# Kernel optimization log

Measured on AMD Instinct MI355X. Metric: run time of the kernel, lower is better.

The kernel has to match this reference:

```python
import jax, jax.numpy as jnp
import numpy as np

silu = jax.nn.silu

B, N, E, H, T, L, A = 8, 20000, 40000, 128, 64, 4, 4


def setup_inputs() -> dict:
    key = jax.random.key(0)
    ks = jax.random.split(key, 20)
    s = 0.05
    w = lambda k, shape: jax.random.normal(k, shape, jnp.float32) * s
    return {
        "x": jax.random.normal(ks[0], (B, N, 3), jnp.float32),
        "t": jax.random.uniform(ks[1], (B,), jnp.float32) * 1000.0,
        "atom_types": jax.random.randint(ks[2], (N,), 0, A),
        "bond_indices": jax.random.randint(ks[3], (E, 2), 0, N),
        "emb_table": w(ks[4], (A, H)),
        "W_t1": w(ks[5], (T, H)), "b_t1": jnp.zeros((H,), jnp.float32),
        "W_t2": w(ks[6], (H, H)), "b_t2": jnp.zeros((H,), jnp.float32),
        "W_node": w(ks[7], (H, H)), "b_node": jnp.zeros((H,), jnp.float32),
        "Wm1": w(ks[8], (L, 2 * H + 1, H)), "bm1": jnp.zeros((L, H), jnp.float32),
        "Wm2": w(ks[9], (L, H, H)), "bm2": jnp.zeros((L, H), jnp.float32),
        "Wn1": w(ks[10], (L, 2 * H, H)), "bn1": jnp.zeros((L, H), jnp.float32),
        "Wn2": w(ks[11], (L, H, H)), "bn2": jnp.zeros((L, H), jnp.float32),
        "Wc1": w(ks[12], (L, H, H)), "bc1": jnp.zeros((L, H), jnp.float32),
        "Wc2": w(ks[13], (L, H, 1)) * 0.001,  # xavier gain=0.001 final coord layer
        "W_o1": w(ks[14], (H, H)), "b_o1": jnp.zeros((H,), jnp.float32),
        "W_o2": w(ks[15], (H, 3)), "b_o2": jnp.zeros((3,), jnp.float32),
    }


def reference(x, t, atom_types, bond_indices, emb_table,
              W_t1, b_t1, W_t2, b_t2, W_node, b_node,
              Wm1, bm1, Wm2, bm2, Wn1, bn1, Wn2, bn2, Wc1, bc1, Wc2,
              W_o1, b_o1, W_o2, b_o2):
    n_atoms = x.shape[1]
    src = bond_indices[:, 0]
    dst = bond_indices[:, 1]

    # sinusoidal time embedding -> time MLP
    half = W_t1.shape[0] // 2
    freq = jnp.exp(jnp.arange(half, dtype=jnp.float32) * (-np.log(10000.0) / (half - 1)))
    te = t[:, None] * freq[None, :]
    te = jnp.concatenate([jnp.sin(te), jnp.cos(te)], axis=-1)  # [B, T]
    t_emb = silu(te @ W_t1 + b_t1) @ W_t2 + b_t2  # [B, H]

    # node init: embedding -> linear -> + time emb
    h0 = emb_table[atom_types] @ W_node + b_node  # [N, H]
    h = h0[None, :, :] + t_emb[:, None, :]  # [B, N, H]

    # degree counts (src+dst incidence), clamped to >=1
    ones = jnp.ones((src.shape[0],), jnp.float32)
    counts = jnp.zeros((n_atoms,), jnp.float32).at[dst].add(ones).at[src].add(ones)
    counts = jnp.maximum(counts, 1.0)

    x_orig = x
    n_layers = Wm1.shape[0]
    for l in range(n_layers):
        h_src = h[:, src, :]
        h_dst = h[:, dst, :]
        coord_diff = x[:, dst, :] - x[:, src, :]  # [B, E, 3]
        dist = jnp.sqrt(jnp.sum(coord_diff * coord_diff, axis=-1, keepdims=True))
        msg_in = jnp.concatenate([h_src, h_dst, dist], axis=-1)  # [B, E, 2H+1]
        m = silu(msg_in @ Wm1[l] + bm1[l])
        m = silu(m @ Wm2[l] + bm2[l])  # [B, E, H]

        agg = jnp.zeros_like(h).at[:, dst, :].add(m).at[:, src, :].add(m)
        h_in = jnp.concatenate([h, agg], axis=-1)
        h = h + silu(h_in @ Wn1[l] + bn1[l]) @ Wn2[l] + bn2[l]

        cw = silu(m @ Wc1[l] + bc1[l]) @ Wc2[l]  # [B, E, 1]
        cdn = coord_diff / (dist + 1e-8)
        upd = cdn * cw
        coord_update = jnp.zeros_like(x).at[:, dst, :].add(upd).at[:, src, :].add(-upd)
        x = x + coord_update / counts[None, :, None]

    coord_change = x - x_orig
    noise_from_h = silu(h @ W_o1 + b_o1) @ W_o2 + b_o2
    return coord_change + noise_from_h
```

## Files before the change

kernel.cpp:

```cpp
#include <hip/hip_runtime.h>
#include <math.h>

#define B_ 8
#define N_ 20000
#define E_ 40000
#define H_ 128
#define L_ 4
#define A_ 4
#define MRS 136
#define EPB 64
#define NPB 64

#define WFENCE __asm__ __volatile__("" ::: "memory")

typedef _Float16 f16x8 __attribute__((ext_vector_type(8)));
typedef _Float16 f16x4v __attribute__((ext_vector_type(4)));
typedef float f32x4 __attribute__((ext_vector_type(4)));

__device__ __forceinline__ float silu_f(float x) {
    return x * __builtin_amdgcn_rcpf(1.f + __expf(-x));
}


__global__ void k_zero(int* __restrict__ deg, int* __restrict__ cursor) {
    int i = blockIdx.x * 256 + threadIdx.x;
    if (i < N_) { deg[i] = 0; cursor[i] = 0; }
}

__global__ void k_deg(const int* __restrict__ bond, int* __restrict__ deg) {
    int e = blockIdx.x * 256 + threadIdx.x;
    if (e < E_) {
        atomicAdd(&deg[bond[2 * e]], 1);
        atomicAdd(&deg[bond[2 * e + 1]], 1);
    }
}

__global__ void k_scan(const int* __restrict__ deg, int* __restrict__ indptr) {
    __shared__ int sums[1024];
    const int CH = (N_ + 1023) / 1024;
    int t = threadIdx.x;
    int s0 = t * CH;
    int s1 = min(s0 + CH, N_);
    int s = 0;
    for (int i = s0; i < s1; ++i) s += deg[i];
    sums[t] = s;
    __syncthreads();
    for (int off = 1; off < 1024; off <<= 1) {
        int v = (t >= off) ? sums[t - off] : 0;
        __syncthreads();
        sums[t] += v;
        __syncthreads();
    }
    int base = (t > 0) ? sums[t - 1] : 0;
    int run = base;
    for (int i = s0; i < s1; ++i) { indptr[i] = run; run += deg[i]; }
    if (s1 == N_ && s0 < N_) indptr[N_] = run;
}

__global__ void k_fill(const int* __restrict__ bond, const int* __restrict__ indptr,
                       int* __restrict__ cursor, int* __restrict__ adj) {
    int e = blockIdx.x * 256 + threadIdx.x;
    if (e < E_) {
        int s = bond[2 * e], d = bond[2 * e + 1];
        int ps = indptr[s] + atomicAdd(&cursor[s], 1);
        adj[ps] = (e << 1);
        int pd = indptr[d] + atomicAdd(&cursor[d], 1);
        adj[pd] = (e << 1) | 1;
    }
}

__global__ void k_wprepL(const float* __restrict__ W, _Float16* __restrict__ Wf,
                         int K, int wstride) {
    int l = blockIdx.y;
    const float* Wl = W + (size_t)l * wstride;
    _Float16* Wfl = Wf + (size_t)l * K * 128;
    int idx = blockIdx.x * 256 + threadIdx.x;
    if (idx >= K * 128) return;
    int j = idx & 7, lane = (idx >> 3) & 63, nt = (idx >> 9) & 7, kt = idx >> 12;
    int k = kt * 32 + (lane >> 4) * 8 + j;
    int n = nt * 16 + (lane & 15);
    Wfl[idx] = (_Float16)Wl[k * 128 + n];
}

__global__ void k_temb(const float* __restrict__ tv,
                       const float* __restrict__ W1, const float* __restrict__ b1,
                       const float* __restrict__ W2, const float* __restrict__ b2,
                       float* __restrict__ t_emb) {
    __shared__ float te[64];
    __shared__ float h1[128];
    int b = blockIdx.x;
    int tid = threadIdx.x;
    float tval = tv[b];
    if (tid < 32) {
        float fr = __expf((float)tid * (-logf(10000.f) / 31.f));
        float a = tval * fr;
        te[tid] = sinf(a);
        te[tid + 32] = cosf(a);
    }
    __syncthreads();
    float acc = b1[tid];
    for (int k = 0; k < 64; ++k) acc += te[k] * W1[k * 128 + tid];
    h1[tid] = silu_f(acc);
    __syncthreads();
    float acc2 = b2[tid];
    for (int k = 0; k < 128; ++k) acc2 += h1[k] * W2[k * 128 + tid];
    t_emb[b * 128 + tid] = acc2;
}

__global__ void k_embproj(const float* __restrict__ emb, const float* __restrict__ W,
                          const float* __restrict__ bias, float* __restrict__ outp) {
    int tid = threadIdx.x;
    int a = tid >> 7, j = tid & 127;
    float acc = bias[j];
    for (int k = 0; k < 128; ++k) acc += emb[a * 128 + k] * W[k * 128 + j];
    outp[a * 128 + j] = acc;
}

__global__ void k_hinit(const int* __restrict__ at, const float* __restrict__ embp,
                        const float* __restrict__ temb, float* __restrict__ h,
                        _Float16* __restrict__ h16) {
    size_t idx4 = (size_t)blockIdx.x * 256 + threadIdx.x;
    size_t e0 = idx4 * 4;
    int j = (int)(e0 % H_);
    size_t bn = e0 / H_;
    int n = (int)(bn % N_);
    int b = (int)(bn / N_);
    int a = at[n];
    float4 ep = *(const float4*)(embp + a * H_ + j);
    float4 tv = *(const float4*)(temb + b * H_ + j);
    float4 r = make_float4(ep.x + tv.x, ep.y + tv.y, ep.z + tv.z, ep.w + tv.w);
    ((float4*)h)[idx4] = r;
    f16x4v o;
    o[0] = (_Float16)r.x; o[1] = (_Float16)r.y; o[2] = (_Float16)r.z; o[3] = (_Float16)r.w;
    *(f16x4v*)(h16 + e0) = o;
}

__global__ void k_xcopy(const float* __restrict__ x, float* __restrict__ xb) {
    int i = blockIdx.x * 256 + threadIdx.x;
    xb[i] = x[i];
}

template <int RS, int KT>
__device__ __forceinline__ void mfma_gemm(const _Float16* Asw, const _Float16* __restrict__ Wf,
                                          f32x4 (&acc)[8], int ml, int quad, int lane) {
    #pragma unroll
    for (int kt = 0; kt < KT; ++kt) {
        f16x8 a = *(const f16x8*)(Asw + ml * RS + kt * 32 + quad * 8);
        #pragma unroll
        for (int nt = 0; nt < 8; ++nt) {
            f16x8 b = *(const f16x8*)(Wf + (((kt * 8 + nt) * 64 + lane) * 8));
            acc[nt] = __builtin_amdgcn_mfma_f32_16x16x32_f16(a, b, acc[nt], 0, 0, 0);
        }
    }
}

template <int RS, int KT>
__device__ __forceinline__ void mfma_gemm2(const _Float16* Asw, const _Float16* __restrict__ Wf,
                                           f32x4 (&acc)[2][8], int ml, int quad, int lane) {
    #pragma unroll
    for (int kt = 0; kt < KT; ++kt) {
        f16x8 a0 = *(const f16x8*)(Asw + ml * RS + kt * 32 + quad * 8);
        f16x8 a1 = *(const f16x8*)(Asw + (16 + ml) * RS + kt * 32 + quad * 8);
        #pragma unroll
        for (int nt = 0; nt < 8; ++nt) {
            f16x8 b = *(const f16x8*)(Wf + (((kt * 8 + nt) * 64 + lane) * 8));
            acc[0][nt] = __builtin_amdgcn_mfma_f32_16x16x32_f16(a0, b, acc[0][nt], 0, 0, 0);
            acc[1][nt] = __builtin_amdgcn_mfma_f32_16x16x32_f16(a1, b, acc[1][nt], 0, 0, 0);
        }
    }
}

__device__ __forceinline__ void load_row(f16x8 (&v)[4], const _Float16* mp) {
    #pragma unroll
    for (int j = 0; j < 4; ++j) v[j] = *(const f16x8*)(mp + j * 8);
}
__device__ __forceinline__ void acc_row(float (&ag)[4][8], const f16x8 (&v)[4]) {
    #pragma unroll
    for (int j = 0; j < 4; ++j)
        #pragma unroll
        for (int i = 0; i < 8; ++i) ag[j][i] += (float)v[j][i];
}


__global__ __launch_bounds__(128, 3) void k_edge_mfma(
    const _Float16* __restrict__ h16, const float* __restrict__ xcur,
    const int* __restrict__ bond,
    const float* __restrict__ Wm1, const float* __restrict__ bm1,
    const _Float16* __restrict__ Wm1f,
    const float* __restrict__ bm2, const _Float16* __restrict__ Wm2f,
    const float* __restrict__ bc1, const _Float16* __restrict__ Wc1f,
    const float* __restrict__ Wc2,
    _Float16* __restrict__ m16, float* __restrict__ upd) {
    __shared__ _Float16 As[EPB * MRS];
    __shared__ float ds_s[EPB];
    __shared__ float dx_s[EPB], dy_s[EPB], dz_s[EPB];
    int tid = threadIdx.x;
    int b = blockIdx.x & 7;
    int e0 = (blockIdx.x >> 3) * EPB;
    size_t be0 = (size_t)b * E_ + e0;

    int el = tid >> 1, q = tid & 1;
    int2 sd = ((const int2*)bond)[e0 + el];
    int s = sd.x, d = sd.y;

    const _Float16* hs = h16 + ((size_t)b * N_ + s) * H_ + q * 64;
    const _Float16* hd = h16 + ((size_t)b * N_ + d) * H_ + q * 64;
    f16x8 ps[8], pd[8];
    #pragma unroll
    for (int j = 0; j < 8; ++j) ps[j] = *(const f16x8*)(hs + j * 8);
    #pragma unroll
    for (int j = 0; j < 8; ++j) pd[j] = *(const f16x8*)(hd + j * 8);
    if (q == 0) {
        const float* xs = xcur + ((size_t)b * N_ + s) * 3;
        const float* xd = xcur + ((size_t)b * N_ + d) * 3;
        float dx = xd[0] - xs[0], dy = xd[1] - xs[1], dz = xd[2] - xs[2];
        ds_s[el] = sqrtf(dx * dx + dy * dy + dz * dz);
        dx_s[el] = dx; dy_s[el] = dy; dz_s[el] = dz;
    }
    {
        _Float16* ap = As + el * MRS + q * 64;
        #pragma unroll
        for (int j = 0; j < 8; ++j) *(f16x8*)(ap + j * 8) = ps[j];
    }
    WFENCE;

    int lane = tid & 63, w = tid >> 6;
    int ml = lane & 15, quad = lane >> 4;
    _Float16* Asw = As + w * 32 * MRS;
    const float* wd = Wm1 + 256 * H_;

    f32x4 acc[2][8];
    #pragma unroll
    for (int nt = 0; nt < 8; ++nt) {
        int col = nt * 16 + ml;
        float bb = bm1[col];
        float ww = wd[col];
        #pragma unroll
        for (int rt = 0; rt < 2; ++rt)
            #pragma unroll
            for (int r = 0; r < 4; ++r)
                acc[rt][nt][r] = bb + ds_s[w * 32 + rt * 16 + quad * 4 + r] * ww;
    }
    mfma_gemm2<MRS, 4>(Asw, Wm1f, acc, ml, quad, lane);
    WFENCE;
    {
        _Float16* ap = As + el * MRS + q * 64;
        #pragma unroll
        for (int j = 0; j < 8; ++j) *(f16x8*)(ap + j * 8) = pd[j];
    }
    WFENCE;
    mfma_gemm2<MRS, 4>(Asw, Wm1f + 4 * 8 * 64 * 8, acc, ml, quad, lane);
    WFENCE;
    #pragma unroll
    for (int rt = 0; rt < 2; ++rt)
        #pragma unroll
        for (int nt = 0; nt < 8; ++nt)
            #pragma unroll
            for (int r = 0; r < 4; ++r)
                Asw[(rt * 16 + quad * 4 + r) * MRS + nt * 16 + ml] = (_Float16)silu_f(acc[rt][nt][r]);
    WFENCE;

    #pragma unroll
    for (int nt = 0; nt < 8; ++nt) {
        float bb = bm2[nt * 16 + ml];
        #pragma unroll
        for (int rt = 0; rt < 2; ++rt)
            #pragma unroll
            for (int r = 0; r < 4; ++r) acc[rt][nt][r] = bb;
    }
    mfma_gemm2<MRS, 4>(Asw, Wm2f, acc, ml, quad, lane);
    WFENCE;
    #pragma unroll
    for (int rt = 0; rt < 2; ++rt)
        #pragma unroll
        for (int nt = 0; nt < 8; ++nt)
            #pragma unroll
            for (int r = 0; r < 4; ++r)
                Asw[(rt * 16 + quad * 4 + r) * MRS + nt * 16 + ml] = (_Float16)silu_f(acc[rt][nt][r]);
    WFENCE;
    #pragma unroll
    for (int j = 0; j < 8; ++j)
        *(f16x8*)(m16 + (be0 + el) * H_ + q * 64 + j * 8) =
            *(const f16x8*)(As + el * MRS + q * 64 + j * 8);

    #pragma unroll
    for (int nt = 0; nt < 8; ++nt) {
        float bb = bc1[nt * 16 + ml];
        #pragma unroll
        for (int rt = 0; rt < 2; ++rt)
            #pragma unroll
            for (int r = 0; r < 4; ++r) acc[rt][nt][r] = bb;
    }
    mfma_gemm2<MRS, 4>(Asw, Wc1f, acc, ml, quad, lane);
    float part[2][4] = {{0.f, 0.f, 0.f, 0.f}, {0.f, 0.f, 0.f, 0.f}};
    #pragma unroll
    for (int nt = 0; nt < 8; ++nt) {
        float wv = Wc2[nt * 16 + ml];
        #pragma unroll
        for (int rt = 0; rt < 2; ++rt)
            #pragma unroll
            for (int r = 0; r < 4; ++r) part[rt][r] += silu_f(acc[rt][nt][r]) * wv;
    }
    #pragma unroll
    for (int off = 1; off < 16; off <<= 1)
        #pragma unroll
        for (int rt = 0; rt < 2; ++rt)
            #pragma unroll
            for (int r = 0; r < 4; ++r) part[rt][r] += __shfl_xor(part[rt][r], off, 64);
    if (ml < 3) {
        #pragma unroll
        for (int rt = 0; rt < 2; ++rt)
            #pragma unroll
            for (int r = 0; r < 4; ++r) {
                int ee = w * 32 + rt * 16 + quad * 4 + r;
                float wv = part[rt][r] * __builtin_amdgcn_rcpf(ds_s[ee] + 1e-8f);
                float comp = (ml == 0) ? dx_s[ee] : ((ml == 1) ? dy_s[ee] : dz_s[ee]);
                upd[(be0 + ee) * 3 + ml] = comp * wv;
            }
    }
}

__global__ void k_coord(const float* __restrict__ xcur, float* __restrict__ xnext,
                        const float* __restrict__ upd,
                        const int* __restrict__ indptr, const int* __restrict__ adj) {
    int idx = blockIdx.x * 256 + threadIdx.x;
    int b = idx / N_;
    int n = idx - b * N_;
    const float* ub = upd + (size_t)b * E_ * 3;
    int p0 = indptr[n], p1 = indptr[n + 1];
    float ax = 0.f, ay = 0.f, az = 0.f;
    for (int p = p0; p < p1; ++p) {
        int a = adj[p];
        int e = a >> 1;
        float sgn = (a & 1) ? 1.f : -1.f;
        ax += sgn * ub[e * 3 + 0];
        ay += sgn * ub[e * 3 + 1];
        az += sgn * ub[e * 3 + 2];
    }
    float rcnt = __builtin_amdgcn_rcpf((float)max(p1 - p0, 1));
    xnext[(size_t)idx * 3 + 0] = xcur[(size_t)idx * 3 + 0] + ax * rcnt;
    xnext[(size_t)idx * 3 + 1] = xcur[(size_t)idx * 3 + 1] + ay * rcnt;
    xnext[(size_t)idx * 3 + 2] = xcur[(size_t)idx * 3 + 2] + az * rcnt;
}

__global__ __launch_bounds__(256, 4) void k_node_mfma(
    float* __restrict__ h, _Float16* __restrict__ h16,
    const _Float16* __restrict__ m16,
    const int* __restrict__ indptr, const int* __restrict__ adj,
    const float* __restrict__ bn1, const _Float16* __restrict__ Wn1f,
    const float* __restrict__ bn2, const _Float16* __restrict__ Wn2f) {
    __shared__ _Float16 As[NPB * MRS];
    int tid = threadIdx.x;
    int el = tid >> 2, q = tid & 3;
    int be = blockIdx.x * NPB + el;
    int b = be / N_, n = be - b * N_;
    {
        const _Float16* hr = h16 + (size_t)be * H_;
        #pragma unroll
        for (int j = 0; j < 4; ++j)
            *(f16x8*)(As + el * MRS + q * 32 + j * 8) = *(const f16x8*)(hr + q * 32 + j * 8);
    }
    int p0 = indptr[n], p1 = indptr[n + 1];
    int d0 = p1 - p0;
    const _Float16* mbb = m16 + (size_t)b * E_ * H_;
    int ea = (d0 > 0) ? (adj[p0] >> 1) : 0;
    int eb = (d0 > 1) ? (adj[p0 + 1] >> 1) : ea;
    f16x8 va[4], vb[4];
    load_row(va, mbb + (size_t)ea * H_ + q * 32);
    load_row(vb, mbb + (size_t)eb * H_ + q * 32);
    WFENCE;

    int lane = tid & 63, w = tid >> 6;
    int ml = lane & 15, quad = lane >> 4;
    _Float16* Asw = As + w * 16 * MRS;
    size_t be0 = (size_t)blockIdx.x * NPB;

    f32x4 acc[8];
    #pragma unroll
    for (int nt = 0; nt < 8; ++nt) {
        float bb = bn1[nt * 16 + ml];
        #pragma unroll
        for (int r = 0; r < 4; ++r) acc[nt][r] = bb;
    }
    mfma_gemm<MRS, 4>(Asw, Wn1f, acc, ml, quad, lane);
    WFENCE;
    {
        float ag[4][8];
        #pragma unroll
        for (int j = 0; j < 4; ++j)
            #pragma unroll
            for (int i = 0; i < 8; ++i) ag[j][i] = 0.f;
        if (d0 > 0) acc_row(ag, va);
        if (d0 > 1) acc_row(ag, vb);
        int p = p0 + 2;
        while (p + 2 <= p1) {
            int e1 = adj[p] >> 1, e2 = adj[p + 1] >> 1;
            f16x8 w1[4], w2[4];
            load_row(w1, mbb + (size_t)e1 * H_ + q * 32);
            load_row(w2, mbb + (size_t)e2 * H_ + q * 32);
            acc_row(ag, w1);
            acc_row(ag, w2);
            p += 2;
        }
        if (p < p1) {
            int e1 = adj[p] >> 1;
            f16x8 w1[4];
            load_row(w1, mbb + (size_t)e1 * H_ + q * 32);
            acc_row(ag, w1);
        }
        #pragma unroll
        for (int j = 0; j < 4; ++j) {
            f16x8 o;
            #pragma unroll
            for (int i = 0; i < 8; ++i) o[i] = (_Float16)ag[j][i];
            *(f16x8*)(As + el * MRS + q * 32 + j * 8) = o;
        }
    }
    WFENCE;
    mfma_gemm<MRS, 4>(Asw, Wn1f + 4 * 8 * 64 * 8, acc, ml, quad, lane);
    WFENCE;
    #pragma unroll
    for (int nt = 0; nt < 8; ++nt)
        #pragma unroll
        for (int r = 0; r < 4; ++r)
            Asw[(quad * 4 + r) * MRS + nt * 16 + ml] = (_Float16)silu_f(acc[nt][r]);
    WFENCE;
    f32x4 acc2[8];
    #pragma unroll
    for (int nt = 0; nt < 8; ++nt) {
        float bb = bn2[nt * 16 + ml];
        #pragma unroll
        for (int r = 0; r < 4; ++r) acc2[nt][r] = bb;
    }
    mfma_gemm<MRS, 4>(Asw, Wn2f, acc2, ml, quad, lane);
    #pragma unroll
    for (int nt = 0; nt < 8; ++nt)
        #pragma unroll
        for (int r = 0; r < 4; ++r) {
            int row = w * 16 + quad * 4 + r;
            size_t g = (size_t)(be0 + row) * H_ + nt * 16 + ml;
            float v = h[g] + acc2[nt][r];
            h[g] = v;
            h16[g] = (_Float16)v;
        }
}

__global__ __launch_bounds__(256, 4) void k_out_mfma(
    const _Float16* __restrict__ h16, const float* __restrict__ xfin, const float* __restrict__ xorig,
    const _Float16* __restrict__ Wo1f, const float* __restrict__ bo1,
    const float* __restrict__ Wo2, const float* __restrict__ bo2,
    float* __restrict__ out) {
    __shared__ _Float16 As[64 * MRS];
    __shared__ float red[64 * 48];
    int tid = threadIdx.x;
    int el = tid >> 2, q = tid & 3;
    size_t be = (size_t)blockIdx.x * 64 + el;
    {
        const _Float16* hr = h16 + be * H_;
        #pragma unroll
        for (int j = 0; j < 4; ++j)
            *(f16x8*)(As + el * MRS + q * 32 + j * 8) = *(const f16x8*)(hr + q * 32 + j * 8);
    }
    WFENCE;

    int lane = tid & 63, w = tid >> 6;
    int ml = lane & 15, quad = lane >> 4;
    _Float16* Asw = As + w * 16 * MRS;

    f32x4 acc[8];
    #pragma unroll
    for (int nt = 0; nt < 8; ++nt) {
        float bb = bo1[nt * 16 + ml];
        #pragma unroll
        for (int r = 0; r < 4; ++r) acc[nt][r] = bb;
    }
    mfma_gemm<MRS, 4>(Asw, Wo1f, acc, ml, quad, lane);
    #pragma unroll
    for (int r = 0; r < 4; ++r) {
        float p0 = 0.f, p1 = 0.f, p2 = 0.f;
        #pragma unroll
        for (int nt = 0; nt < 8; ++nt) {
            float u = silu_f(acc[nt][r]);
            int col = nt * 16 + ml;
            p0 += u * Wo2[col * 3 + 0];
            p1 += u * Wo2[col * 3 + 1];
            p2 += u * Wo2[col * 3 + 2];
        }
        int row = w * 16 + quad * 4 + r;
        red[row * 48 + ml * 3 + 0] = p0;
        red[row * 48 + ml * 3 + 1] = p1;
        red[row * 48 + ml * 3 + 2] = p2;
    }
    __syncthreads();
    if (tid < 192) {
        int row = tid / 3, jj = tid - row * 3;
        float s = 0.f;
        #pragma unroll
        for (int cc = 0; cc < 16; ++cc) s += red[row * 48 + cc * 3 + jj];
        size_t grow = (size_t)blockIdx.x * 64 + row;
        out[grow * 3 + jj] = s + bo2[jj] + xfin[grow * 3 + jj] - xorig[grow * 3 + jj];
    }
}


extern "C" void kernel_launch(void* const* d_in, const int* in_sizes, int n_in,
                              void* d_out, int out_size, void* d_ws, size_t ws_size,
                              hipStream_t stream) {
    const float* x = (const float*)d_in[0];
    const float* t = (const float*)d_in[1];
    const int* atom_types = (const int*)d_in[2];
    const int* bond = (const int*)d_in[3];
    const float* emb_table = (const float*)d_in[4];
    const float* W_t1 = (const float*)d_in[5];
    const float* b_t1 = (const float*)d_in[6];
    const float* W_t2 = (const float*)d_in[7];
    const float* b_t2 = (const float*)d_in[8];
    const float* W_node = (const float*)d_in[9];
    const float* b_node = (const float*)d_in[10];
    const float* Wm1 = (const float*)d_in[11];
    const float* bm1 = (const float*)d_in[12];
    const float* Wm2 = (const float*)d_in[13];
    const float* bm2 = (const float*)d_in[14];
    const float* Wn1 = (const float*)d_in[15];
    const float* bn1 = (const float*)d_in[16];
    const float* Wn2 = (const float*)d_in[17];
    const float* bn2 = (const float*)d_in[18];
    const float* Wc1 = (const float*)d_in[19];
    const float* bc1 = (const float*)d_in[20];
    const float* Wc2 = (const float*)d_in[21];
    const float* W_o1 = (const float*)d_in[22];
    const float* b_o1 = (const float*)d_in[23];
    const float* W_o2 = (const float*)d_in[24];
    const float* b_o2 = (const float*)d_in[25];
    float* out = (float*)d_out;

    char* p = (char*)d_ws;
    auto alloc = [&](size_t bytes) -> void* {
        void* r = (void*)p;
        p += (bytes + 255) & ~(size_t)255;
        return r;
    };
    float* t_emb = (float*)alloc((size_t)B_ * H_ * 4);
    float* emb_proj = (float*)alloc((size_t)A_ * H_ * 4);
    int* deg = (int*)alloc((size_t)N_ * 4);
    int* indptr = (int*)alloc((size_t)(N_ + 1) * 4);
    int* cursor = (int*)alloc((size_t)N_ * 4);
    int* adj = (int*)alloc((size_t)2 * E_ * 4);
    float* xb0 = (float*)alloc((size_t)B_ * N_ * 3 * 4);
    float* xb1 = (float*)alloc((size_t)B_ * N_ * 3 * 4);
    float* upd = (float*)alloc((size_t)B_ * E_ * 3 * 4);
    float* h = (float*)alloc((size_t)B_ * N_ * H_ * 4);
    _Float16* h16 = (_Float16*)alloc((size_t)B_ * N_ * H_ * 2);
    _Float16* m16 = (_Float16*)alloc((size_t)B_ * E_ * H_ * 2);
    _Float16* Wm1f = (_Float16*)alloc((size_t)L_ * 256 * H_ * 2);
    _Float16* Wm2f = (_Float16*)alloc((size_t)L_ * H_ * H_ * 2);
    _Float16* Wc1f = (_Float16*)alloc((size_t)L_ * H_ * H_ * 2);
    _Float16* Wn1f = (_Float16*)alloc((size_t)L_ * 256 * H_ * 2);
    _Float16* Wn2f = (_Float16*)alloc((size_t)L_ * H_ * H_ * 2);
    _Float16* Wo1f = (_Float16*)alloc((size_t)H_ * H_ * 2);

    k_zero<<<(N_ + 255) / 256, 256, 0, stream>>>(deg, cursor);
    k_deg<<<(E_ + 255) / 256, 256, 0, stream>>>(bond, deg);
    k_scan<<<1, 1024, 0, stream>>>(deg, indptr);
    k_fill<<<(E_ + 255) / 256, 256, 0, stream>>>(bond, indptr, cursor, adj);
    k_temb<<<B_, 128, 0, stream>>>(t, W_t1, b_t1, W_t2, b_t2, t_emb);
    k_embproj<<<1, 512, 0, stream>>>(emb_table, W_node, b_node, emb_proj);
    k_hinit<<<(B_ * N_ * H_ / 4) / 256, 256, 0, stream>>>(atom_types, emb_proj, t_emb, h, h16);
    k_xcopy<<<(B_ * N_ * 3) / 256, 256, 0, stream>>>(x, xb0);
    k_wprepL<<<dim3(128, L_), 256, 0, stream>>>(Wm1, Wm1f, 256, 257 * H_);
    k_wprepL<<<dim3(64, L_), 256, 0, stream>>>(Wm2, Wm2f, 128, H_ * H_);
    k_wprepL<<<dim3(64, L_), 256, 0, stream>>>(Wc1, Wc1f, 128, H_ * H_);
    k_wprepL<<<dim3(128, L_), 256, 0, stream>>>(Wn1, Wn1f, 256, 2 * H_ * H_);
    k_wprepL<<<dim3(64, L_), 256, 0, stream>>>(Wn2, Wn2f, 128, H_ * H_);
    k_wprepL<<<dim3(64, 1), 256, 0, stream>>>(W_o1, Wo1f, 128, H_ * H_);

    float* xc = xb0;
    float* xn = xb1;
    for (int l = 0; l < L_; ++l) {
        k_edge_mfma<<<(B_ * E_) / EPB, 128, 0, stream>>>(
            h16, xc, bond,
            Wm1 + (size_t)l * 257 * H_, bm1 + l * H_, Wm1f + (size_t)l * 256 * H_,
            bm2 + l * H_, Wm2f + (size_t)l * H_ * H_,
            bc1 + l * H_, Wc1f + (size_t)l * H_ * H_,
            Wc2 + (size_t)l * H_, m16, upd);
        k_coord<<<(B_ * N_) / 256, 256, 0, stream>>>(xc, xn, upd, indptr, adj);
        k_node_mfma<<<(B_ * N_) / NPB, 256, 0, stream>>>(
            h, h16, m16, indptr, adj,
            bn1 + l * H_, Wn1f + (size_t)l * 256 * H_,
            bn2 + l * H_, Wn2f + (size_t)l * H_ * H_);
        float* tmp = xc; xc = xn; xn = tmp;
    }
    k_out_mfma<<<(B_ * N_) / 64, 256, 0, stream>>>(h16, xc, x, Wo1f, b_o1, W_o2, b_o2, out);
}
```

Baseline: 973.2 us.

## Fuse coordinate update into node kernel and coalesce edge update stores via LDS

Removes the separate k_coord launch per layer. The per-node coordinate gather over the adjacency list now runs inside k_node_mfma on one of four threads per node, placed before the node GEMMs to overlap its latency. The edge kernel stages per-edge coordinate updates in shared memory and writes them out contiguously, replacing strided per-lane stores. This saves launch overhead and gives better store coalescing, at the cost of extra registers and serial per-thread adjacency loops inside the node kernel.

```diff
diff --git a/kernel.cpp b/kernel.cpp
--- a/kernel.cpp
+++ b/kernel.cpp
@@ -194,6 +194,7 @@
     __shared__ _Float16 As[EPB * MRS];
     __shared__ float ds_s[EPB];
     __shared__ float dx_s[EPB], dy_s[EPB], dz_s[EPB];
+    __shared__ float u_s[EPB * 3];
     int tid = threadIdx.x;
     int b = blockIdx.x & 7;
     int e0 = (blockIdx.x >> 3) * EPB;
@@ -315,37 +316,22 @@
                 int ee = w * 32 + rt * 16 + quad * 4 + r;
                 float wv = part[rt][r] * __builtin_amdgcn_rcpf(ds_s[ee] + 1e-8f);
                 float comp = (ml == 0) ? dx_s[ee] : ((ml == 1) ? dy_s[ee] : dz_s[ee]);
-                upd[(be0 + ee) * 3 + ml] = comp * wv;
+                u_s[ee * 3 + ml] = comp * wv;
             }
     }
-}
-
-__global__ void k_coord(const float* __restrict__ xcur, float* __restrict__ xnext,
-                        const float* __restrict__ upd,
-                        const int* __restrict__ indptr, const int* __restrict__ adj) {
-    int idx = blockIdx.x * 256 + threadIdx.x;
-    int b = idx / N_;
-    int n = idx - b * N_;
-    const float* ub = upd + (size_t)b * E_ * 3;
-    int p0 = indptr[n], p1 = indptr[n + 1];
-    float ax = 0.f, ay = 0.f, az = 0.f;
-    for (int p = p0; p < p1; ++p) {
-        int a = adj[p];
-        int e = a >> 1;
-        float sgn = (a & 1) ? 1.f : -1.f;
-        ax += sgn * ub[e * 3 + 0];
-        ay += sgn * ub[e * 3 + 1];
-        az += sgn * ub[e * 3 + 2];
-    }
-    float rcnt = __builtin_amdgcn_rcpf((float)max(p1 - p0, 1));
-    xnext[(size_t)idx * 3 + 0] = xcur[(size_t)idx * 3 + 0] + ax * rcnt;
-    xnext[(size_t)idx * 3 + 1] = xcur[(size_t)idx * 3 + 1] + ay * rcnt;
-    xnext[(size_t)idx * 3 + 2] = xcur[(size_t)idx * 3 + 2] + az * rcnt;
+    WFENCE;
+    {
+        float* up = upd + (be0 + w * 32) * 3;
+        up[lane] = u_s[w * 96 + lane];
+        if (lane < 32) up[64 + lane] = u_s[w * 96 + 64 + lane];
+    }
 }
 
 __global__ __launch_bounds__(256, 4) void k_node_mfma(
     float* __restrict__ h, _Float16* __restrict__ h16,
     const _Float16* __restrict__ m16,
+    const float* __restrict__ upd,
+    const float* __restrict__ xcur, float* __restrict__ xnext,
     const int* __restrict__ indptr, const int* __restrict__ adj,
     const float* __restrict__ bn1, const _Float16* __restrict__ Wn1f,
     const float* __restrict__ bn2, const _Float16* __restrict__ Wn2f) {
@@ -417,6 +403,18 @@
         }
     }
     WFENCE;
+    float cx = 0.f, cy = 0.f, cz = 0.f;
+    if (q == 0) {
+        const float* ub = upd + (size_t)b * E_ * 3;
+        for (int p = p0; p < p1; ++p) {
+            int a = adj[p];
+            int e = a >> 1;
+            float sgn = (a & 1) ? 1.f : -1.f;
+            cx += sgn * ub[e * 3 + 0];
+            cy += sgn * ub[e * 3 + 1];
+            cz += sgn * ub[e * 3 + 2];
+        }
+    }
     mfma_gemm<MRS, 4>(Asw, Wn1f + 4 * 8 * 64 * 8, acc, ml, quad, lane);
     WFENCE;
     #pragma unroll
@@ -433,6 +431,12 @@
         for (int r = 0; r < 4; ++r) acc2[nt][r] = bb;
     }
     mfma_gemm<MRS, 4>(Asw, Wn2f, acc2, ml, quad, lane);
+    if (q == 0) {
+        float rcnt = __builtin_amdgcn_rcpf((float)max(d0, 1));
+        xnext[(size_t)be * 3 + 0] = xcur[(size_t)be * 3 + 0] + cx * rcnt;
+        xnext[(size_t)be * 3 + 1] = xcur[(size_t)be * 3 + 1] + cy * rcnt;
+        xnext[(size_t)be * 3 + 2] = xcur[(size_t)be * 3 + 2] + cz * rcnt;
+    }
     #pragma unroll
     for (int nt = 0; nt < 8; ++nt)
         #pragma unroll
@@ -583,9 +587,8 @@
             bm2 + l * H_, Wm2f + (size_t)l * H_ * H_,
             bc1 + l * H_, Wc1f + (size_t)l * H_ * H_,
             Wc2 + (size_t)l * H_, m16, upd);
-        k_coord<<<(B_ * N_) / 256, 256, 0, stream>>>(xc, xn, upd, indptr, adj);
         k_node_mfma<<<(B_ * N_) / NPB, 256, 0, stream>>>(
-            h, h16, m16, indptr, adj,
+            h, h16, m16, upd, xc, xn, indptr, adj,
             bn1 + l * H_, Wn1f + (size_t)l * 256 * H_,
             bn2 + l * H_, Wn2f + (size_t)l * H_ * H_);
         float* tmp = xc; xc = xn; xn = tmp;
```

Result: slower. 993.1 us (+2.0%).
